# Optimization experiments

Hardware: AMD Instinct MI355X
Metric: run time of the kernel (lower is better)

The kernel has to match this reference:

```python
import jax, jax.numpy as jnp
import numpy as np

LN_EPS = 1e-5


def setup_inputs() -> dict:
    key = jax.random.key(0)
    ks = jax.random.split(key, 5)
    N, E, D = 50000, 600000, 128
    x = jax.random.normal(ks[0], (N, D), dtype=jnp.float32)
    edge_index = jax.random.randint(ks[1], (2, E), 0, N, dtype=jnp.int64)
    W_l = jax.random.normal(ks[2], (D, D), dtype=jnp.float32) * (1.0 / np.sqrt(D))
    b_l = jnp.zeros((D,), dtype=jnp.float32)
    W_r = jax.random.normal(ks[3], (D, D), dtype=jnp.float32) * (1.0 / np.sqrt(D))
    gamma = jnp.ones((D,), dtype=jnp.float32)
    beta = jnp.zeros((D,), dtype=jnp.float32)
    return {"x": x, "edge_index": edge_index, "W_l": W_l, "b_l": b_l,
            "W_r": W_r, "gamma": gamma, "beta": beta}


def reference(x, edge_index, W_l, b_l, W_r, gamma, beta):
    # SAGEConv (mean aggregation): out = lin_l(mean_{j in N(i)} x_j) + lin_r(x_i)
    N = x.shape[0]
    src, dst = edge_index[0], edge_index[1]
    msg = x[src]                                                # (E, D) gather
    agg = jax.ops.segment_sum(msg, dst, num_segments=N)         # (N, D) scatter-add
    cnt = jax.ops.segment_sum(jnp.ones_like(dst, dtype=x.dtype), dst, num_segments=N)
    mean = agg / jnp.maximum(cnt, 1.0)[:, None]
    h = mean @ W_l.T + b_l + x @ W_r.T                          # (N, D)
    # LayerNorm over feature dim
    mu = jnp.mean(h, axis=-1, keepdims=True)
    var = jnp.mean(jnp.square(h - mu), axis=-1, keepdims=True)
    h = (h - mu) * jax.lax.rsqrt(var + LN_EPS) * gamma + beta
    # ReLU; Dropout is identity in eval mode
    return jax.nn.relu(h)
```

## Files before the change

kernel.cpp:

```cpp
#include <hip/hip_runtime.h>
#include <stdint.h>

#define DIM 128
#define LN_EPS 1e-5f
#define ELLW 64
#define ELLS 63
#define ATS 264
#define PINIT ((int)0xAAAAAAAA)

typedef __attribute__((ext_vector_type(8))) short bf16x8;
typedef __attribute__((ext_vector_type(4))) float f32x4;

static __device__ __forceinline__ uint16_t f2bf(float f) {
    uint32_t u = __float_as_uint(f);
    return (uint16_t)((u + 0x7fffu + ((u >> 16) & 1u)) >> 16);
}

__global__ __launch_bounds__(256) void prep_kernel(
    const int* __restrict__ ei,
    const float* __restrict__ Wl,
    const float* __restrict__ Wr,
    int* __restrict__ ell, int* __restrict__ novf, int* __restrict__ ovf,
    uint16_t* __restrict__ wc, int E)
{
    int tid = blockIdx.x * blockDim.x + threadIdx.x;
    int nth = gridDim.x * blockDim.x;
    for (int e = tid; e < E; e += nth) {
        int src = ei[e];
        int dst = ei[E + e];
        int* row = ell + (size_t)dst * ELLW;
        int r = atomicAdd(row, 1) - PINIT;
        if (r >= 0 && r < ELLS) {
            row[1 + r] = src;
        } else if (r >= ELLS) {
            int q = atomicAdd(novf, 1) - PINIT;
            if (q >= 0 && q < E) {
                ovf[2 * q] = dst;
                ovf[2 * q + 1] = src;
            }
        }
    }
    for (int i = tid; i < DIM * 256; i += nth) {
        int d = i >> 8, k = i & 255;
        float v = (k < DIM) ? Wl[d * DIM + k] : Wr[d * DIM + (k - DIM)];
        wc[i] = f2bf(v);
    }
}

__global__ __launch_bounds__(256, 4) void fused_kernel(
    const float* __restrict__ x,
    const int* __restrict__ ell,
    const int* __restrict__ novf,
    const int* __restrict__ ovf,
    const uint16_t* __restrict__ wc,
    const float* __restrict__ bl,
    const float* __restrict__ gma,
    const float* __restrict__ bta,
    float* __restrict__ out,
    int N, int E)
{
    __shared__ uint16_t atile[2][16 * ATS];
    __shared__ float pln[2][16][2][2];

    const int lane = threadIdx.x & 63;
    const int w    = threadIdx.x >> 6;
    const int p    = w >> 1;
    const int h    = w & 1;
    const int tile_row0 = blockIdx.x * 32 + p * 16;
    const int grow0     = tile_row0 + h * 8;

    int dg_s[8], nell[8], mx = 0;
    #pragma unroll
    for (int r = 0; r < 8; ++r) {
        int row = grow0 + r;
        int d = (row < N)
            ? (__builtin_amdgcn_readfirstlane(ell[(size_t)row * ELLW]) - PINIT)
            : 0;
        d = (d < 0) ? 0 : d;
        dg_s[r] = d;
        int t = d < ELLS ? d : ELLS;
        nell[r] = t;
        mx = (t > mx) ? t : mx;
    }

    int sidx[8];
    #pragma unroll
    for (int r = 0; r < 8; ++r)
        sidx[r] = (lane < nell[r]) ? ell[(size_t)(grow0 + r) * ELLW + 1 + lane] : 0;

    float m0[8], m1[8];
    #pragma unroll
    for (int r = 0; r < 8; ++r) { m0[r] = 0.0f; m1[r] = 0.0f; }

    for (int j = 0; j < mx; ++j) {
        #pragma unroll
        for (int r = 0; r < 8; ++r) {
            float pr = (j < nell[r]) ? 1.0f : 0.0f;
            int s = __builtin_amdgcn_readlane(sidx[r], j);
            const float* xr = x + (size_t)s * DIM;
            m0[r] = fmaf(pr, xr[lane], m0[r]);
            m1[r] = fmaf(pr, xr[lane + 64], m1[r]);
        }
    }

    {
        int no = __builtin_amdgcn_readfirstlane(novf[0]) - PINIT;
        no = (no < 0) ? 0 : (no > E ? E : no);
        for (int i = 0; i < no; ++i) {
            int dsto = __builtin_amdgcn_readfirstlane(ovf[2 * i]);
            int srco = __builtin_amdgcn_readfirstlane(ovf[2 * i + 1]);
            if (dsto >= grow0 && dsto < grow0 + 8) {
                const float* xr = x + (size_t)srco * DIM;
                float v0 = xr[lane], v1 = xr[lane + 64];
                #pragma unroll
                for (int r = 0; r < 8; ++r) {
                    float pr = (dsto == grow0 + r) ? 1.0f : 0.0f;
                    m0[r] = fmaf(pr, v0, m0[r]);
                    m1[r] = fmaf(pr, v1, m1[r]);
                }
            }
        }
    }

    {
        uint16_t* at = atile[p];
        #pragma unroll
        for (int r = 0; r < 8; ++r) {
            int row = grow0 + r;
            int rr = (row < N) ? row : 0;
            float rc = (dg_s[r] > 0) ? (1.0f / (float)dg_s[r]) : 0.0f;
            const float* xw = x + (size_t)rr * DIM;
            int lr = h * 8 + r;
            at[lr * ATS + lane]       = f2bf(m0[r] * rc);
            at[lr * ATS + 64 + lane]  = f2bf(m1[r] * rc);
            at[lr * ATS + 128 + lane] = f2bf(xw[lane]);
            at[lr * ATS + 192 + lane] = f2bf(xw[lane + 64]);
        }
    }
    __syncthreads();

    const int nsub = lane & 15;
    const int quad = lane >> 4;
    const uint16_t* at = atile[p];

    f32x4 acc[4];
    #pragma unroll
    for (int tt = 0; tt < 4; ++tt) {
        float b = bl[(h * 4 + tt) * 16 + nsub];
        acc[tt] = (f32x4){b, b, b, b};
    }

    #pragma unroll
    for (int c = 0; c < 8; ++c) {
        bf16x8 af = *(const bf16x8*)&at[nsub * ATS + c * 32 + quad * 8];
        #pragma unroll
        for (int tt = 0; tt < 4; ++tt) {
            int tg = h * 4 + tt;
            bf16x8 bfr = *(const bf16x8*)&wc[(size_t)(tg * 16 + nsub) * 256 + c * 32 + quad * 8];
            acc[tt] = __builtin_amdgcn_mfma_f32_16x16x32_bf16(af, bfr, acc[tt], 0, 0, 0);
        }
    }

    #pragma unroll
    for (int i = 0; i < 4; ++i) {
        float s = 0.0f, q = 0.0f;
        #pragma unroll
        for (int tt = 0; tt < 4; ++tt) {
            float v = acc[tt][i];
            s += v;
            q += v * v;
        }
        #pragma unroll
        for (int off = 1; off < 16; off <<= 1) {
            s += __shfl_xor(s, off, 64);
            q += __shfl_xor(q, off, 64);
        }
        if (nsub == 0) {
            pln[p][quad * 4 + i][h][0] = s;
            pln[p][quad * 4 + i][h][1] = q;
        }
    }
    __syncthreads();

    #pragma unroll
    for (int i = 0; i < 4; ++i) {
        int lrow = quad * 4 + i;
        float s = pln[p][lrow][0][0] + pln[p][lrow][1][0];
        float q = pln[p][lrow][0][1] + pln[p][lrow][1][1];
        float mu = s * (1.0f / 128.0f);
        float var = q * (1.0f / 128.0f) - mu * mu;
        float rs = rsqrtf(fmaxf(var, 0.0f) + LN_EPS);
        int grow = tile_row0 + lrow;
        if (grow < N) {
            float* op = out + (size_t)grow * DIM;
            #pragma unroll
            for (int tt = 0; tt < 4; ++tt) {
                int f = (h * 4 + tt) * 16 + nsub;
                float o = fmaxf((acc[tt][i] - mu) * rs * gma[f] + bta[f], 0.0f);
                op[f] = o;
            }
        }
    }
}

extern "C" void kernel_launch(void* const* d_in, const int* in_sizes, int n_in,
                              void* d_out, int out_size, void* d_ws, size_t ws_size,
                              hipStream_t stream) {
    const float* x  = (const float*)d_in[0];
    const int* ei   = (const int*)d_in[1];
    const float* Wl = (const float*)d_in[2];
    const float* bl = (const float*)d_in[3];
    const float* Wr = (const float*)d_in[4];
    const float* ga = (const float*)d_in[5];
    const float* be = (const float*)d_in[6];
    float* out = (float*)d_out;

    int N = in_sizes[0] / DIM;
    int E = in_sizes[1] / 2;

    int* ell      = (int*)d_ws;
    int* novf     = ell + (size_t)N * ELLW;
    uint16_t* wc  = (uint16_t*)(novf + 16);
    int* ovf      = (int*)(wc + DIM * 256);

    prep_kernel<<<(E + 255) / 256, 256, 0, stream>>>(
        ei, Wl, Wr, ell, novf, ovf, wc, E);

    {
        int blocks = (N + 31) / 32;
        fused_kernel<<<blocks, 256, 0, stream>>>(
            x, ell, novf, ovf, wc, bl, ga, be, out, N, E);
    }
}
```

Measured before the change: 191.0 us.

## Gather neighbor features from a bf16 copy of x and shrink ELL width

The prep kernel now writes a packed bf16 copy of x. The fused kernel gathers neighbor rows and self rows from that copy, halving the bytes each random gather pulls. The ELL row width drops from 64 to 32 slots, which shrinks the adjacency workspace and the row-header traffic, and the prep kernel handles edges in pairs using vector loads. The cost is an extra full pass over x to convert it, plus aggregating the mean from bf16-rounded inputs, which adds some rounding error before the bf16 MFMA.

```diff
diff --git a/kernel.cpp b/kernel.cpp
--- a/kernel.cpp
+++ b/kernel.cpp
@@ -3,8 +3,8 @@
 
 #define DIM 128
 #define LN_EPS 1e-5f
-#define ELLW 64
-#define ELLS 63
+#define ELLW 32
+#define ELLS 31
 #define ATS 264
 #define PINIT ((int)0xAAAAAAAA)
 
@@ -14,32 +14,65 @@
 static __device__ __forceinline__ uint16_t f2bf(float f) {
     uint32_t u = __float_as_uint(f);
     return (uint16_t)((u + 0x7fffu + ((u >> 16) & 1u)) >> 16);
+}
+static __device__ __forceinline__ float bf_lo(uint32_t w) {
+    return __uint_as_float(w << 16);
+}
+static __device__ __forceinline__ float bf_hi(uint32_t w) {
+    return __uint_as_float(w & 0xffff0000u);
 }
 
 __global__ __launch_bounds__(256) void prep_kernel(
     const int* __restrict__ ei,
     const float* __restrict__ Wl,
     const float* __restrict__ Wr,
+    const float* __restrict__ x,
     int* __restrict__ ell, int* __restrict__ novf, int* __restrict__ ovf,
-    uint16_t* __restrict__ wc, int E)
+    uint16_t* __restrict__ wc, uint16_t* __restrict__ x16,
+    int E, int N)
 {
     int tid = blockIdx.x * blockDim.x + threadIdx.x;
     int nth = gridDim.x * blockDim.x;
-    for (int e = tid; e < E; e += nth) {
-        int src = ei[e];
-        int dst = ei[E + e];
-        int* row = ell + (size_t)dst * ELLW;
-        int r = atomicAdd(row, 1) - PINIT;
-        if (r >= 0 && r < ELLS) {
-            row[1 + r] = src;
-        } else if (r >= ELLS) {
-            int q = atomicAdd(novf, 1) - PINIT;
-            if (q >= 0 && q < E) {
-                ovf[2 * q] = dst;
-                ovf[2 * q + 1] = src;
-            }
-        }
-    }
+
+    int npair = (E + 1) >> 1;
+    for (int pe = tid; pe < npair; pe += nth) {
+        int e0 = 2 * pe;
+        if (e0 + 1 < E) {
+            int2 s2 = *(const int2*)(ei + e0);
+            int2 d2 = *(const int2*)(ei + E + e0);
+            int* row0 = ell + (size_t)d2.x * ELLW;
+            int* row1 = ell + (size_t)d2.y * ELLW;
+            int r0 = atomicAdd(row0, 1) - PINIT;
+            int r1 = atomicAdd(row1, 1) - PINIT;
+            if (r0 >= 0 && r0 < ELLS) row0[1 + r0] = s2.x;
+            else if (r0 >= ELLS) {
+                int q = atomicAdd(novf, 1) - PINIT;
+                if (q >= 0 && q < E) { ovf[2 * q] = d2.x; ovf[2 * q + 1] = s2.x; }
+            }
+            if (r1 >= 0 && r1 < ELLS) row1[1 + r1] = s2.y;
+            else if (r1 >= ELLS) {
+                int q = atomicAdd(novf, 1) - PINIT;
+                if (q >= 0 && q < E) { ovf[2 * q] = d2.y; ovf[2 * q + 1] = s2.y; }
+            }
+        } else if (e0 < E) {
+            int src = ei[e0], dst = ei[E + e0];
+            int* row = ell + (size_t)dst * ELLW;
+            int r = atomicAdd(row, 1) - PINIT;
+            if (r >= 0 && r < ELLS) row[1 + r] = src;
+            else if (r >= ELLS) {
+                int q = atomicAdd(novf, 1) - PINIT;
+                if (q >= 0 && q < E) { ovf[2 * q] = dst; ovf[2 * q + 1] = src; }
+            }
+        }
+    }
+
+    int nxp = (N * DIM) >> 1;
+    for (int i = tid; i < nxp; i += nth) {
+        float2 v = *(const float2*)(x + 2 * i);
+        uint32_t u = ((uint32_t)f2bf(v.y) << 16) | (uint32_t)f2bf(v.x);
+        ((uint32_t*)x16)[i] = u;
+    }
+
     for (int i = tid; i < DIM * 256; i += nth) {
         int d = i >> 8, k = i & 255;
         float v = (k < DIM) ? Wl[d * DIM + k] : Wr[d * DIM + (k - DIM)];
@@ -48,7 +81,7 @@
 }
 
 __global__ __launch_bounds__(256, 4) void fused_kernel(
-    const float* __restrict__ x,
+    const uint16_t* __restrict__ x16,
     const int* __restrict__ ell,
     const int* __restrict__ novf,
     const int* __restrict__ ovf,
@@ -97,9 +130,9 @@
         for (int r = 0; r < 8; ++r) {
             float pr = (j < nell[r]) ? 1.0f : 0.0f;
             int s = __builtin_amdgcn_readlane(sidx[r], j);
-            const float* xr = x + (size_t)s * DIM;
-            m0[r] = fmaf(pr, xr[lane], m0[r]);
-            m1[r] = fmaf(pr, xr[lane + 64], m1[r]);
+            uint32_t u = *(const uint32_t*)(x16 + (size_t)s * DIM + 2 * lane);
+            m0[r] = fmaf(pr, bf_lo(u), m0[r]);
+            m1[r] = fmaf(pr, bf_hi(u), m1[r]);
         }
     }
 
@@ -110,8 +143,8 @@
             int dsto = __builtin_amdgcn_readfirstlane(ovf[2 * i]);
             int srco = __builtin_amdgcn_readfirstlane(ovf[2 * i + 1]);
             if (dsto >= grow0 && dsto < grow0 + 8) {
-                const float* xr = x + (size_t)srco * DIM;
-                float v0 = xr[lane], v1 = xr[lane + 64];
+                uint32_t u = *(const uint32_t*)(x16 + (size_t)srco * DIM + 2 * lane);
+                float v0 = bf_lo(u), v1 = bf_hi(u);
                 #pragma unroll
                 for (int r = 0; r < 8; ++r) {
                     float pr = (dsto == grow0 + r) ? 1.0f : 0.0f;
@@ -129,12 +162,13 @@
             int row = grow0 + r;
             int rr = (row < N) ? row : 0;
             float rc = (dg_s[r] > 0) ? (1.0f / (float)dg_s[r]) : 0.0f;
-            const float* xw = x + (size_t)rr * DIM;
             int lr = h * 8 + r;
-            at[lr * ATS + lane]       = f2bf(m0[r] * rc);
-            at[lr * ATS + 64 + lane]  = f2bf(m1[r] * rc);
-            at[lr * ATS + 128 + lane] = f2bf(xw[lane]);
-            at[lr * ATS + 192 + lane] = f2bf(xw[lane + 64]);
+            ushort2 mu2;
+            mu2.x = f2bf(m0[r] * rc);
+            mu2.y = f2bf(m1[r] * rc);
+            *(ushort2*)&at[lr * ATS + 2 * lane] = mu2;
+            uint32_t xv = *(const uint32_t*)(x16 + (size_t)rr * DIM + 2 * lane);
+            *(uint32_t*)&at[lr * ATS + 128 + 2 * lane] = xv;
         }
     }
     __syncthreads();
@@ -221,14 +255,15 @@
     int* ell      = (int*)d_ws;
     int* novf     = ell + (size_t)N * ELLW;
     uint16_t* wc  = (uint16_t*)(novf + 16);
-    int* ovf      = (int*)(wc + DIM * 256);
-
-    prep_kernel<<<(E + 255) / 256, 256, 0, stream>>>(
-        ei, Wl, Wr, ell, novf, ovf, wc, E);
+    uint16_t* x16 = wc + DIM * 256;
+    int* ovf      = (int*)(x16 + (size_t)N * DIM);
+
+    prep_kernel<<<(E / 2 + 255) / 256, 256, 0, stream>>>(
+        ei, Wl, Wr, x, ell, novf, ovf, wc, x16, E, N);
 
     {
         int blocks = (N + 31) / 32;
         fused_kernel<<<blocks, 256, 0, stream>>>(
-            x, ell, novf, ovf, wc, bl, ga, be, out, N, E);
-    }
-}
+            x16, ell, novf, ovf, wc, bl, ga, be, out, N, E);
+    }
+}
```

Result: no change. 192.6 us (+0.9%).
